# Kernel tuning notes

Measured on AMD Instinct MI355X. Metric: run time of the kernel, lower is better.

The kernel has to match this reference:

```python
import jax, jax.numpy as jnp
import numpy as np
import math

NUM_HEADS = 12


def setup_inputs() -> dict:
    key = jax.random.key(0)
    ks = jax.random.split(key, 9)
    R, L, B, E = 128, 512, 1, 768
    s = 1.0 / math.sqrt(E)
    return {
        "x": jax.random.normal(ks[0], (R, L, B, E), dtype=jnp.float32),
        "wq": jax.random.normal(ks[1], (E, E), dtype=jnp.float32) * s,
        "bq": jax.random.normal(ks[2], (E,), dtype=jnp.float32) * 0.02,
        "wk": jax.random.normal(ks[3], (E, E), dtype=jnp.float32) * s,
        "bk": jax.random.normal(ks[4], (E,), dtype=jnp.float32) * 0.02,
        "wv": jax.random.normal(ks[5], (E, E), dtype=jnp.float32) * s,
        "bv": jax.random.normal(ks[6], (E,), dtype=jnp.float32) * 0.02,
        "wo": jax.random.normal(ks[7], (E, E), dtype=jnp.float32) * s,
        "bo": jax.random.normal(ks[8], (E,), dtype=jnp.float32) * 0.02,
    }


def reference(x, wq, bq, wk, bk, wv, bv, wo, bo):
    # x: [num_rows, num_cols, batch, embed_dim]
    R, L, B, E = x.shape
    H = NUM_HEADS
    D = E // H
    # scaling = head_dim**-0.5 / sqrt(num_rows)  (align_scaling)
    scaling = (D ** -0.5) / math.sqrt(R)

    q = (x @ wq.T + bq).reshape(R, L, B, H, D) * scaling
    k = (x @ wk.T + bk).reshape(R, L, B, H, D)
    v = (x @ wv.T + bv).reshape(R, L, B, H, D)

    # row attention: contract over rows r and head_dim d -> logits [h, n, i, j]
    attn_weights = jnp.einsum("rinhd,rjnhd->hnij", q, k)
    attn_probs = jax.nn.softmax(attn_weights, axis=-1)

    context = jnp.einsum("hnij,rjnhd->rinhd", attn_probs, v)
    context = context.reshape(R, L, B, E)
    output = context @ wo.T + bo
    return (output, attn_probs)
```

## Files before the change

### kernel.cpp

```cpp
#include <hip/hip_runtime.h>
#include <hip/hip_bf16.h>

typedef unsigned short u16;
typedef u16   u16x4 __attribute__((ext_vector_type(4)));
typedef u16   u16x8 __attribute__((ext_vector_type(8)));
typedef short bf16x8 __attribute__((ext_vector_type(8)));
typedef float f32x4 __attribute__((ext_vector_type(4)));

#define R_    128
#define L_    512
#define E_    768
#define H_    12
#define RD_   8192
#define M_    65536
#define OUT0_N 50331648
#define PART_ 3145728

__device__ __forceinline__ u16 rne_bf16(float f) {
  unsigned u = __builtin_bit_cast(unsigned, f);
  u += 0x7FFFu + ((u >> 16) & 1u);
  return (u16)(u >> 16);
}

__device__ __forceinline__ void gload_lds16(const u16* g, u16* l) {
  __builtin_amdgcn_global_load_lds(
      (const __attribute__((address_space(1))) void*)g,
      (__attribute__((address_space(3))) void*)l, 16, 0, 0);
}

__device__ __forceinline__ int xcd_remap(int d, int nwg) {
  return (d & 7) * (nwg >> 3) + (d >> 3);
}

__device__ __forceinline__ void gemm_core256(
    const u16* __restrict__ Ab, const u16* __restrict__ Bb,
    const int lda, const int ldb, const int K,
    u16* sm, f32x4 acc[8][4])
{
  const int t    = threadIdx.x;
  const int lane = t & 63;
  const int w    = t >> 6;
  const int wm   = (w >> 2) << 7;
  const int wn   = (w & 3) << 6;
  const int frow = lane & 15;

  const int crow  = t >> 3;
  const int gslot = (t & 7) ^ (crow & 7);
  const u16* gA = Ab + (size_t)crow * lda + (gslot << 3);
  const u16* gB = Bb + (size_t)crow * ldb + (gslot << 3);
  const int stg = t << 3;

  const int rd0 = (((lane >> 4)    ) ^ (lane & 7)) << 3;
  const int rd1 = (((lane >> 4) | 4) ^ (lane & 7)) << 3;

#define STG_A(c_, buf_, ko_) \
  gload_lds16(gA + (ko_) + (size_t)((c_) << 6) * lda, (buf_) + ((c_) << 12) + stg)
#define STG_B(c_, buf_, ko_) \
  gload_lds16(gB + (ko_) + (size_t)((c_) << 6) * ldb, (buf_) + 16384 + ((c_) << 12) + stg)

  const int nt = K >> 6;
  STG_B(0, sm, 0); STG_B(1, sm, 0); STG_B(2, sm, 0); STG_B(3, sm, 0);
  STG_A(0, sm, 0); STG_A(2, sm, 0); STG_A(1, sm, 0); STG_A(3, sm, 0);
  asm volatile("s_waitcnt vmcnt(2)" ::: "memory");
  __builtin_amdgcn_s_barrier();

  for (int tt = 0; tt < nt; ++tt) {
    u16* bufc = sm + ((tt & 1) << 15);
    u16* bufn = sm + (((tt + 1) & 1) << 15);
    const bool st = (tt + 1 < nt);
    const int ko = (tt + 1) << 6;

    bf16x8 af[4], bff[4];
#pragma unroll
    for (int b = 0; b < 4; ++b)
      bff[b] = *(const bf16x8*)(bufc + 16384 + ((wn + b * 16 + frow) << 6) + rd0);
#pragma unroll
    for (int a = 0; a < 4; ++a)
      af[a] = *(const bf16x8*)(bufc + ((wm + a * 16 + frow) << 6) + rd0);
    if (st) { STG_B(0, bufn, ko); STG_B(1, bufn, ko); }
    __builtin_amdgcn_s_barrier();
    __builtin_amdgcn_s_setprio(1);
#pragma unroll
    for (int a = 0; a < 4; ++a)
#pragma unroll
      for (int b = 0; b < 4; ++b)
        acc[a][b] = __builtin_amdgcn_mfma_f32_16x16x32_bf16(af[a], bff[b], acc[a][b], 0, 0, 0);
    __builtin_amdgcn_s_setprio(0);
    if (st) asm volatile("s_waitcnt vmcnt(2)" ::: "memory");
    else    asm volatile("s_waitcnt vmcnt(0)" ::: "memory");
    __builtin_amdgcn_s_barrier();

#pragma unroll
    for (int a = 0; a < 4; ++a)
      af[a] = *(const bf16x8*)(bufc + ((wm + (a + 4) * 16 + frow) << 6) + rd0);
    if (st) { STG_B(2, bufn, ko); STG_B(3, bufn, ko); }
    __builtin_amdgcn_s_barrier();
    __builtin_amdgcn_s_setprio(1);
#pragma unroll
    for (int a = 0; a < 4; ++a)
#pragma unroll
      for (int b = 0; b < 4; ++b)
        acc[a + 4][b] = __builtin_amdgcn_mfma_f32_16x16x32_bf16(af[a], bff[b], acc[a + 4][b], 0, 0, 0);
    __builtin_amdgcn_s_setprio(0);
    __builtin_amdgcn_s_barrier();

#pragma unroll
    for (int b = 0; b < 4; ++b)
      bff[b] = *(const bf16x8*)(bufc + 16384 + ((wn + b * 16 + frow) << 6) + rd1);
#pragma unroll
    for (int a = 0; a < 4; ++a)
      af[a] = *(const bf16x8*)(bufc + ((wm + a * 16 + frow) << 6) + rd1);
    if (st) { STG_A(0, bufn, ko); STG_A(2, bufn, ko); }
    __builtin_amdgcn_s_barrier();
    __builtin_amdgcn_s_setprio(1);
#pragma unroll
    for (int a = 0; a < 4; ++a)
#pragma unroll
      for (int b = 0; b < 4; ++b)
        acc[a][b] = __builtin_amdgcn_mfma_f32_16x16x32_bf16(af[a], bff[b], acc[a][b], 0, 0, 0);
    __builtin_amdgcn_s_setprio(0);
    __builtin_amdgcn_s_barrier();

#pragma unroll
    for (int a = 0; a < 4; ++a)
      af[a] = *(const bf16x8*)(bufc + ((wm + (a + 4) * 16 + frow) << 6) + rd1);
    if (st) { STG_A(1, bufn, ko); STG_A(3, bufn, ko); }
    __builtin_amdgcn_s_barrier();
    __builtin_amdgcn_s_setprio(1);
#pragma unroll
    for (int a = 0; a < 4; ++a)
#pragma unroll
      for (int b = 0; b < 4; ++b)
        acc[a + 4][b] = __builtin_amdgcn_mfma_f32_16x16x32_bf16(af[a], bff[b], acc[a + 4][b], 0, 0, 0);
    __builtin_amdgcn_s_setprio(0);
    if (st) asm volatile("s_waitcnt vmcnt(2)" ::: "memory");
    __builtin_amdgcn_s_barrier();
  }
#undef STG_A
#undef STG_B
}

#define EPILOGUE_IDX256                           \
  const int lane = threadIdx.x & 63;              \
  const int w    = threadIdx.x >> 6;              \
  const int wm   = (w >> 2) << 7;                 \
  const int wn   = (w & 3) << 6;                  \
  const int row4 = (lane >> 4) << 2;              \
  const int coll = lane & 15;

#define ACC_INIT256                               \
  f32x4 acc[8][4];                                \
  {                                               \
    f32x4 zz = {0.0f, 0.0f, 0.0f, 0.0f};          \
    _Pragma("unroll")                             \
    for (int a = 0; a < 8; ++a)                   \
      _Pragma("unroll")                           \
      for (int b = 0; b < 4; ++b) acc[a][b] = zz; \
  }

__device__ __forceinline__ void gemm_core(
    const u16* __restrict__ Ab, const u16* __restrict__ Bb,
    const int lda, const int ldb, const int K,
    u16* sm, f32x4 acc[4][4])
{
  const int t    = threadIdx.x;
  const int lane = t & 63;
  const int w    = t >> 6;
  const int wm   = (w >> 1) << 6;
  const int wn   = (w & 1) << 6;
  const int frow = lane & 15;

  const int srow = (w << 3) + (lane >> 3);
  const int scol = ((lane & 7) ^ (lane >> 3)) << 3;
  const u16* gA = Ab + (size_t)srow * lda + scol;
  const u16* gB = Bb + (size_t)srow * ldb + scol;
  const int stg_l = (w << 9) + (lane << 3);

#pragma unroll
  for (int j = 0; j < 4; ++j) {
    gload_lds16(gA + (size_t)(j << 5) * lda, sm + (j << 11) + stg_l);
    gload_lds16(gB + (size_t)(j << 5) * ldb, sm + 8192 + (j << 11) + stg_l);
  }

  const int nt = K >> 6;
  for (int tt = 0; tt < nt; ++tt) {
    const int cur = tt & 1;
    u16* bufc = sm + (cur << 14);
    u16* bufn = sm + ((cur ^ 1) << 14);
    __builtin_amdgcn_s_barrier();
    if (tt + 1 < nt) {
      const u16* gA1 = gA + ((size_t)(tt + 1) << 6);
      const u16* gB1 = gB + ((size_t)(tt + 1) << 6);
#pragma unroll
      for (int j = 0; j < 4; ++j) {
        gload_lds16(gA1 + (size_t)(j << 5) * lda, bufn + (j << 11) + stg_l);
        gload_lds16(gB1 + (size_t)(j << 5) * ldb, bufn + 8192 + (j << 11) + stg_l);
      }
      asm volatile("s_waitcnt vmcnt(8)" ::: "memory");
    } else {
      asm volatile("s_waitcnt vmcnt(0)" ::: "memory");
    }
    __builtin_amdgcn_s_barrier();
    const u16* sA = bufc;
    const u16* sB = bufc + 8192;
#pragma unroll
    for (int kk = 0; kk < 2; ++kk) {
      const int rdcol = (((kk << 2) + (lane >> 4)) ^ (lane & 7)) << 3;
      bf16x8 af[4], bff[4];
#pragma unroll
      for (int a = 0; a < 4; ++a)
        af[a] = *(const bf16x8*)(sA + ((wm + a * 16 + frow) << 6) + rdcol);
#pragma unroll
      for (int b = 0; b < 4; ++b)
        bff[b] = *(const bf16x8*)(sB + ((wn + b * 16 + frow) << 6) + rdcol);
#pragma unroll
      for (int a = 0; a < 4; ++a)
#pragma unroll
        for (int b = 0; b < 4; ++b)
          acc[a][b] = __builtin_amdgcn_mfma_f32_16x16x32_bf16(af[a], bff[b], acc[a][b], 0, 0, 0);
    }
  }
}

#define EPILOGUE_IDX                              \
  const int lane = threadIdx.x & 63;              \
  const int w    = threadIdx.x >> 6;              \
  const int wm   = (w >> 1) << 6;                 \
  const int wn   = (w & 1) << 6;                  \
  const int row4 = (lane >> 4) << 2;              \
  const int coll = lane & 15;

#define ACC_INIT                                  \
  f32x4 acc[4][4];                                \
  {                                               \
    f32x4 zz = {0.0f, 0.0f, 0.0f, 0.0f};          \
    _Pragma("unroll")                             \
    for (int a = 0; a < 4; ++a)                   \
      _Pragma("unroll")                           \
      for (int b = 0; b < 4; ++b) acc[a][b] = zz; \
  }

__global__ __launch_bounds__(512) void k_gemm_qkv(
    const u16* __restrict__ xbf, const u16* __restrict__ wqkv,
    const float* __restrict__ bq, const float* __restrict__ bk,
    const float* __restrict__ bv,
    u16* __restrict__ qt, u16* __restrict__ kt, u16* __restrict__ vt2,
    const float scaling)
{
  __shared__ __align__(16) u16 smem[65536];
  const int d0 = blockIdx.x + 9 * blockIdx.y;
  const int l  = xcd_remap(d0, 2304);
  const int bn = l % 9;
  const int bm = l / 9;
  ACC_INIT256;
  gemm_core256(xbf + (size_t)bm * 256 * E_, wqkv + (size_t)bn * 256 * E_,
               E_, E_, E_, smem, acc);
  EPILOGUE_IDX256;
  const int which = bn / 3;
  const int c0 = (bn % 3) << 8;
  const float* bias = (which == 0) ? bq : (which == 1) ? bk : bv;

  if (which < 2) {
    u16* dst = (which == 0) ? qt : kt;
    const float mult = (which == 0) ? scaling : 1.0f;
#pragma unroll
    for (int a = 0; a < 8; ++a) {
#pragma unroll
      for (int b = 0; b < 4; ++b) {
        const int c = c0 + wn + b * 16 + coll;
        const int h = c >> 6, d = c & 63;
        const float bias_v = bias[c];
#pragma unroll
        for (int r = 0; r < 4; ++r) {
          const int m = (bm << 8) + wm + a * 16 + row4 + r;
          const int rr = m >> 9, i = m & 511;
          const float v = (acc[a][b][r] + bias_v) * mult;
          dst[((size_t)(h * 512 + i) << 13) + (rr << 6) + d] = rne_bf16(v);
        }
      }
    }
  } else {
    const int rr = bm >> 1;
    const int j0 = (bm & 1) << 8;
    const int wq4 = w & 3;
    for (int p = 0; p < 4; ++p) {
      __syncthreads();
      if (wq4 == p) {
#pragma unroll
        for (int a = 0; a < 8; ++a) {
          const int ml = wm + a * 16 + row4;
#pragma unroll
          for (int b = 0; b < 4; ++b) {
            const int c = c0 + wn + b * 16 + coll;
            const int nl = b * 16 + coll;
            const float bias_v = bias[c];
            u16x4 pk;
#pragma unroll
            for (int r = 0; r < 4; ++r) pk[r] = rne_bf16(acc[a][b][r] + bias_v);
            *(u16x4*)(smem + nl * 264 + ml) = pk;
          }
        }
      }
      __syncthreads();
      for (int idx = threadIdx.x; idx < 2048; idx += 512) {
        const int nl = idx >> 5, seg = idx & 31;
        const int c = c0 + (p << 6) + nl;
        const int h = c >> 6, d = c & 63;
        u16x8 vdat = *(const u16x8*)(smem + nl * 264 + (seg << 3));
        *(u16x8*)(vt2 + ((size_t)((h << 13) + (rr << 6) + d) << 9) + j0 + (seg << 3)) = vdat;
      }
    }
  }
}

__global__ __launch_bounds__(256) void k_gemm_logits(
    const u16* __restrict__ qt, const u16* __restrict__ kt,
    float* __restrict__ lgp)
{
  __shared__ __align__(16) u16 smem[32768];
  const int d0 = blockIdx.x + 4 * blockIdx.y + 16 * blockIdx.z;
  const int l  = xcd_remap(d0, 768);
  const int bm = l & 3, bn = (l >> 2) & 3;
  const int hk = l >> 4;
  const int h  = hk >> 2, ks = hk & 3;
  ACC_INIT;
  const u16* A = qt + ((size_t)h << 22) + ((size_t)bm << 20) + (ks << 11);
  const u16* B = kt + ((size_t)h << 22) + ((size_t)bn << 20) + (ks << 11);
  gemm_core(A, B, RD_, RD_, 2048, smem, acc);
  EPILOGUE_IDX;
  float* dst = lgp + ((size_t)(ks * 12 + h) << 18);
#pragma unroll
  for (int a = 0; a < 4; ++a)
#pragma unroll
    for (int b = 0; b < 4; ++b) {
      const int j = bn * 128 + wn + b * 16 + coll;
#pragma unroll
      for (int r = 0; r < 4; ++r) {
        const int i = bm * 128 + wm + a * 16 + row4 + r;
        dst[((size_t)i << 9) + j] = acc[a][b][r];
      }
    }
}

__global__ __launch_bounds__(256) void k_softmax(
    const float* __restrict__ lgp, float* __restrict__ probs,
    u16* __restrict__ pbf)
{
  const int row = blockIdx.x;
  const size_t base = (size_t)row << 9;
  const int t = threadIdx.x;
  const int lane = t & 63, w = t >> 6;
  float x0 = (lgp[base + t]       + lgp[PART_ + base + t])
           + (lgp[2 * (size_t)PART_ + base + t]       + lgp[3 * (size_t)PART_ + base + t]);
  float x1 = (lgp[base + t + 256] + lgp[PART_ + base + t + 256])
           + (lgp[2 * (size_t)PART_ + base + t + 256] + lgp[3 * (size_t)PART_ + base + t + 256]);
  float m = fmaxf(x0, x1);
#pragma unroll
  for (int off = 32; off > 0; off >>= 1) m = fmaxf(m, __shfl_xor(m, off, 64));
  __shared__ float red[8];
  if (lane == 0) red[w] = m;
  __syncthreads();
  m = fmaxf(fmaxf(red[0], red[1]), fmaxf(red[2], red[3]));
  float e0 = __expf(x0 - m), e1 = __expf(x1 - m);
  float s = e0 + e1;
#pragma unroll
  for (int off = 32; off > 0; off >>= 1) s += __shfl_xor(s, off, 64);
  if (lane == 0) red[4 + w] = s;
  __syncthreads();
  s = (red[4] + red[5]) + (red[6] + red[7]);
  const float inv = 1.0f / s;
  const float p0 = e0 * inv, p1 = e1 * inv;
  probs[base + t] = p0;
  probs[base + t + 256] = p1;
  pbf[base + t]       = rne_bf16(p0);
  pbf[base + t + 256] = rne_bf16(p1);
}

__global__ __launch_bounds__(512) void k_gemm_ctx(
    const u16* __restrict__ pbf, const u16* __restrict__ vt2,
    u16* __restrict__ ctx)
{
  __shared__ __align__(16) u16 smem[65536];
  const int d0 = blockIdx.x + (blockIdx.y << 6);
  const int l  = xcd_remap(d0, 768);
  const int bm = l & 1, bn = (l >> 1) & 31, h = l >> 6;
  ACC_INIT256;
  const u16* A = pbf + ((size_t)h << 18) + ((size_t)bm << 17);
  const u16* B = vt2 + ((size_t)h << 22) + ((size_t)bn << 17);
  gemm_core256(A, B, 512, 512, 512, smem, acc);
  EPILOGUE_IDX256;
#pragma unroll
  for (int a = 0; a < 8; ++a)
#pragma unroll
    for (int b = 0; b < 4; ++b) {
      const int n = (bn << 8) + wn + b * 16 + coll;
      const int rr = n >> 6, d = n & 63;
#pragma unroll
      for (int r = 0; r < 4; ++r) {
        const int i = (bm << 8) + wm + a * 16 + row4 + r;
        ctx[(size_t)((rr << 9) + i) * E_ + (h << 6) + d] = rne_bf16(acc[a][b][r]);
      }
    }
}

__global__ __launch_bounds__(512) void k_gemm_out(
    const u16* __restrict__ ctx, const u16* __restrict__ wob,
    const float* __restrict__ bo, float* __restrict__ out0)
{
  __shared__ __align__(16) u16 smem[65536];
  const int d0 = blockIdx.x + 3 * blockIdx.y;
  const int l  = xcd_remap(d0, 768);
  const int bn = l % 3;
  const int bm = l / 3;
  ACC_INIT256;
  gemm_core256(ctx + (size_t)bm * 256 * E_, wob + (size_t)bn * 256 * E_,
               E_, E_, E_, smem, acc);
  EPILOGUE_IDX256;
#pragma unroll
  for (int a = 0; a < 8; ++a)
#pragma unroll
    for (int b = 0; b < 4; ++b) {
      const int n = (bn << 8) + wn + b * 16 + coll;
      const float bias_v = bo[n];
#pragma unroll
      for (int r = 0; r < 4; ++r) {
        const int m = (bm << 8) + wm + a * 16 + row4 + r;
        out0[(size_t)m * E_ + n] = acc[a][b][r] + bias_v;
      }
    }
}

__device__ __forceinline__ u16x4 cvt4(float4 v) {
  u16x4 o;
  o.x = rne_bf16(v.x); o.y = rne_bf16(v.y);
  o.z = rne_bf16(v.z); o.w = rne_bf16(v.w);
  return o;
}

__global__ __launch_bounds__(256) void k_cvt_all(
    const float4* __restrict__ x,
    const float4* __restrict__ wq, const float4* __restrict__ wk,
    const float4* __restrict__ wv, const float4* __restrict__ wo,
    u16x4* __restrict__ xbf, u16x4* __restrict__ wqkv, u16x4* __restrict__ wob)
{
  const int n4x = OUT0_N / 4;
  const int n4w = (E_ * E_) / 4;
  const int stride = gridDim.x * blockDim.x;
  for (int i = blockIdx.x * blockDim.x + threadIdx.x; i < n4x; i += stride) {
    xbf[i] = cvt4(x[i]);
    if (i < n4w) {
      wqkv[i]          = cvt4(wq[i]);
      wqkv[n4w + i]    = cvt4(wk[i]);
      wqkv[2 * n4w + i] = cvt4(wv[i]);
      wob[i]           = cvt4(wo[i]);
    }
  }
}

__global__ void k_ws_too_small(float* out0) {
  if (threadIdx.x == 0 && blockIdx.x == 0) out0[0] = 1.0e9f;
}

extern "C" void kernel_launch(void* const* d_in, const int* in_sizes, int n_in,
                              void* d_out, int out_size, void* d_ws, size_t ws_size,
                              hipStream_t stream)
{
  const float* x  = (const float*)d_in[0];
  const float* wq = (const float*)d_in[1];
  const float* bq = (const float*)d_in[2];
  const float* wk = (const float*)d_in[3];
  const float* bk = (const float*)d_in[4];
  const float* wv = (const float*)d_in[5];
  const float* bv = (const float*)d_in[6];
  const float* wo = (const float*)d_in[7];
  const float* bo = (const float*)d_in[8];

  float* out0 = (float*)d_out;
  float* outp = out0 + (size_t)OUT0_N;

  const size_t off_xbf   = 0;
  const size_t off_qt    = 100663296;
  const size_t off_kt    = 201326592;
  const size_t off_vt    = 301989888;
  const size_t off_pbf   = 402653184;
  const size_t off_wqkv  = 408944640;
  const size_t off_wob   = 412483584;
  const size_t need      = 413663232;

  if (ws_size < need) {
    k_ws_too_small<<<1, 64, 0, stream>>>(out0);
    return;
  }

  char* ws = (char*)d_ws;
  u16* xbf  = (u16*)(ws + off_xbf);
  float* lgp = (float*)(ws + off_xbf);
  u16* qt   = (u16*)(ws + off_qt);
  u16* kt   = (u16*)(ws + off_kt);
  u16* vt2  = (u16*)(ws + off_vt);
  u16* pbf  = (u16*)(ws + off_pbf);
  u16* wqkv = (u16*)(ws + off_wqkv);
  u16* wob  = (u16*)(ws + off_wob);

  const float scaling = 0.011048543456039806f;

  k_cvt_all<<<2048, 256, 0, stream>>>((const float4*)x,
                                      (const float4*)wq, (const float4*)wk,
                                      (const float4*)wv, (const float4*)wo,
                                      (u16x4*)xbf, (u16x4*)wqkv, (u16x4*)wob);
  k_gemm_qkv<<<dim3(9, 256), 512, 0, stream>>>(xbf, wqkv, bq, bk, bv,
                                               qt, kt, vt2, scaling);
  k_gemm_logits<<<dim3(4, 4, 48), 256, 0, stream>>>(qt, kt, lgp);
  k_softmax<<<6144, 256, 0, stream>>>(lgp, outp, pbf);
  k_gemm_ctx<<<dim3(64, 12), 512, 0, stream>>>(pbf, vt2, xbf );
  k_gemm_out<<<dim3(3, 256), 512, 0, stream>>>(xbf, wob, bo, out0);
}
```

Before: 601.8 us.

## Use 16 waves per 256x256 GEMM tile with simpler double-buffered K loop

The 256x256 GEMM core goes from 8 waves, each computing 128x64, to 16 waves (1024 threads), each computing 64x64. Accumulator registers per wave are halved. The finely interleaved staged load/compute schedule is replaced by one prefetch of the next K tile at the top of each iteration, followed by two k-substeps of MFMA. The aim is more waves to hide latency with less register pressure, at the cost of losing the fine-grained load/compute interleave, and launch_bounds(1024,4) may squeeze registers.

```diff
diff --git a/kernel.cpp b/kernel.cpp
--- a/kernel.cpp
+++ b/kernel.cpp
@@ -35,12 +35,12 @@
 __device__ __forceinline__ void gemm_core256(
     const u16* __restrict__ Ab, const u16* __restrict__ Bb,
     const int lda, const int ldb, const int K,
-    u16* sm, f32x4 acc[8][4])
+    u16* sm, f32x4 acc[4][4])
 {
   const int t    = threadIdx.x;
   const int lane = t & 63;
   const int w    = t >> 6;
-  const int wm   = (w >> 2) << 7;
+  const int wm   = (w >> 2) << 6;
   const int wn   = (w & 3) << 6;
   const int frow = lane & 15;
 
@@ -54,86 +54,47 @@
   const int rd1 = (((lane >> 4) | 4) ^ (lane & 7)) << 3;
 
 #define STG_A(c_, buf_, ko_) \
-  gload_lds16(gA + (ko_) + (size_t)((c_) << 6) * lda, (buf_) + ((c_) << 12) + stg)
+  gload_lds16(gA + (ko_) + (size_t)((c_) << 7) * lda, (buf_) + ((c_) << 13) + stg)
 #define STG_B(c_, buf_, ko_) \
-  gload_lds16(gB + (ko_) + (size_t)((c_) << 6) * ldb, (buf_) + 16384 + ((c_) << 12) + stg)
+  gload_lds16(gB + (ko_) + (size_t)((c_) << 7) * ldb, (buf_) + 16384 + ((c_) << 13) + stg)
 
   const int nt = K >> 6;
-  STG_B(0, sm, 0); STG_B(1, sm, 0); STG_B(2, sm, 0); STG_B(3, sm, 0);
-  STG_A(0, sm, 0); STG_A(2, sm, 0); STG_A(1, sm, 0); STG_A(3, sm, 0);
-  asm volatile("s_waitcnt vmcnt(2)" ::: "memory");
+  STG_A(0, sm, 0); STG_A(1, sm, 0); STG_B(0, sm, 0); STG_B(1, sm, 0);
+  asm volatile("s_waitcnt vmcnt(0)" ::: "memory");
   __builtin_amdgcn_s_barrier();
 
   for (int tt = 0; tt < nt; ++tt) {
     u16* bufc = sm + ((tt & 1) << 15);
     u16* bufn = sm + (((tt + 1) & 1) << 15);
     const bool st = (tt + 1 < nt);
-    const int ko = (tt + 1) << 6;
+    if (st) {
+      const int ko = (tt + 1) << 6;
+      STG_A(0, bufn, ko); STG_A(1, bufn, ko);
+      STG_B(0, bufn, ko); STG_B(1, bufn, ko);
+      asm volatile("s_waitcnt vmcnt(4)" ::: "memory");
+    } else {
+      asm volatile("s_waitcnt vmcnt(0)" ::: "memory");
+    }
+    __builtin_amdgcn_s_barrier();
 
     bf16x8 af[4], bff[4];
 #pragma unroll
-    for (int b = 0; b < 4; ++b)
-      bff[b] = *(const bf16x8*)(bufc + 16384 + ((wn + b * 16 + frow) << 6) + rd0);
-#pragma unroll
-    for (int a = 0; a < 4; ++a)
-      af[a] = *(const bf16x8*)(bufc + ((wm + a * 16 + frow) << 6) + rd0);
-    if (st) { STG_B(0, bufn, ko); STG_B(1, bufn, ko); }
-    __builtin_amdgcn_s_barrier();
-    __builtin_amdgcn_s_setprio(1);
-#pragma unroll
-    for (int a = 0; a < 4; ++a)
+    for (int kk = 0; kk < 2; ++kk) {
+      const int rdk = kk ? rd1 : rd0;
+#pragma unroll
+      for (int a = 0; a < 4; ++a)
+        af[a] = *(const bf16x8*)(bufc + ((wm + a * 16 + frow) << 6) + rdk);
 #pragma unroll
       for (int b = 0; b < 4; ++b)
-        acc[a][b] = __builtin_amdgcn_mfma_f32_16x16x32_bf16(af[a], bff[b], acc[a][b], 0, 0, 0);
-    __builtin_amdgcn_s_setprio(0);
-    if (st) asm volatile("s_waitcnt vmcnt(2)" ::: "memory");
-    else    asm volatile("s_waitcnt vmcnt(0)" ::: "memory");
-    __builtin_amdgcn_s_barrier();
-
-#pragma unroll
-    for (int a = 0; a < 4; ++a)
-      af[a] = *(const bf16x8*)(bufc + ((wm + (a + 4) * 16 + frow) << 6) + rd0);
-    if (st) { STG_B(2, bufn, ko); STG_B(3, bufn, ko); }
-    __builtin_amdgcn_s_barrier();
-    __builtin_amdgcn_s_setprio(1);
-#pragma unroll
-    for (int a = 0; a < 4; ++a)
-#pragma unroll
-      for (int b = 0; b < 4; ++b)
-        acc[a + 4][b] = __builtin_amdgcn_mfma_f32_16x16x32_bf16(af[a], bff[b], acc[a + 4][b], 0, 0, 0);
-    __builtin_amdgcn_s_setprio(0);
-    __builtin_amdgcn_s_barrier();
-
-#pragma unroll
-    for (int b = 0; b < 4; ++b)
-      bff[b] = *(const bf16x8*)(bufc + 16384 + ((wn + b * 16 + frow) << 6) + rd1);
-#pragma unroll
-    for (int a = 0; a < 4; ++a)
-      af[a] = *(const bf16x8*)(bufc + ((wm + a * 16 + frow) << 6) + rd1);
-    if (st) { STG_A(0, bufn, ko); STG_A(2, bufn, ko); }
-    __builtin_amdgcn_s_barrier();
-    __builtin_amdgcn_s_setprio(1);
-#pragma unroll
-    for (int a = 0; a < 4; ++a)
-#pragma unroll
-      for (int b = 0; b < 4; ++b)
-        acc[a][b] = __builtin_amdgcn_mfma_f32_16x16x32_bf16(af[a], bff[b], acc[a][b], 0, 0, 0);
-    __builtin_amdgcn_s_setprio(0);
-    __builtin_amdgcn_s_barrier();
-
-#pragma unroll
-    for (int a = 0; a < 4; ++a)
-      af[a] = *(const bf16x8*)(bufc + ((wm + (a + 4) * 16 + frow) << 6) + rd1);
-    if (st) { STG_A(1, bufn, ko); STG_A(3, bufn, ko); }
-    __builtin_amdgcn_s_barrier();
-    __builtin_amdgcn_s_setprio(1);
-#pragma unroll
-    for (int a = 0; a < 4; ++a)
-#pragma unroll
-      for (int b = 0; b < 4; ++b)
-        acc[a + 4][b] = __builtin_amdgcn_mfma_f32_16x16x32_bf16(af[a], bff[b], acc[a + 4][b], 0, 0, 0);
-    __builtin_amdgcn_s_setprio(0);
-    if (st) asm volatile("s_waitcnt vmcnt(2)" ::: "memory");
+        bff[b] = *(const bf16x8*)(bufc + 16384 + ((wn + b * 16 + frow) << 6) + rdk);
+      __builtin_amdgcn_s_setprio(1);
+#pragma unroll
+      for (int a = 0; a < 4; ++a)
+#pragma unroll
+        for (int b = 0; b < 4; ++b)
+          acc[a][b] = __builtin_amdgcn_mfma_f32_16x16x32_bf16(af[a], bff[b], acc[a][b], 0, 0, 0);
+      __builtin_amdgcn_s_setprio(0);
+    }
     __builtin_amdgcn_s_barrier();
   }
 #undef STG_A
@@ -143,17 +104,17 @@
 #define EPILOGUE_IDX256                           \
   const int lane = threadIdx.x & 63;              \
   const int w    = threadIdx.x >> 6;              \
-  const int wm   = (w >> 2) << 7;                 \
+  const int wm   = (w >> 2) << 6;                 \
   const int wn   = (w & 3) << 6;                  \
   const int row4 = (lane >> 4) << 2;              \
   const int coll = lane & 15;
 
 #define ACC_INIT256                               \
-  f32x4 acc[8][4];                                \
+  f32x4 acc[4][4];                                \
   {                                               \
     f32x4 zz = {0.0f, 0.0f, 0.0f, 0.0f};          \
     _Pragma("unroll")                             \
-    for (int a = 0; a < 8; ++a)                   \
+    for (int a = 0; a < 4; ++a)                   \
       _Pragma("unroll")                           \
       for (int b = 0; b < 4; ++b) acc[a][b] = zz; \
   }
@@ -240,7 +201,7 @@
       for (int b = 0; b < 4; ++b) acc[a][b] = zz; \
   }
 
-__global__ __launch_bounds__(512) void k_gemm_qkv(
+__global__ __launch_bounds__(1024, 4) void k_gemm_qkv(
     const u16* __restrict__ xbf, const u16* __restrict__ wqkv,
     const float* __restrict__ bq, const float* __restrict__ bk,
     const float* __restrict__ bv,
@@ -264,7 +225,7 @@
     u16* dst = (which == 0) ? qt : kt;
     const float mult = (which == 0) ? scaling : 1.0f;
 #pragma unroll
-    for (int a = 0; a < 8; ++a) {
+    for (int a = 0; a < 4; ++a) {
 #pragma unroll
       for (int b = 0; b < 4; ++b) {
         const int c = c0 + wn + b * 16 + coll;
@@ -287,7 +248,7 @@
       __syncthreads();
       if (wq4 == p) {
 #pragma unroll
-        for (int a = 0; a < 8; ++a) {
+        for (int a = 0; a < 4; ++a) {
           const int ml = wm + a * 16 + row4;
 #pragma unroll
           for (int b = 0; b < 4; ++b) {
@@ -302,7 +263,7 @@
         }
       }
       __syncthreads();
-      for (int idx = threadIdx.x; idx < 2048; idx += 512) {
+      for (int idx = threadIdx.x; idx < 2048; idx += 1024) {
         const int nl = idx >> 5, seg = idx & 31;
         const int c = c0 + (p << 6) + nl;
         const int h = c >> 6, d = c & 63;
@@ -376,7 +337,7 @@
   pbf[base + t + 256] = rne_bf16(p1);
 }
 
-__global__ __launch_bounds__(512) void k_gemm_ctx(
+__global__ __launch_bounds__(1024, 4) void k_gemm_ctx(
     const u16* __restrict__ pbf, const u16* __restrict__ vt2,
     u16* __restrict__ ctx)
 {
@@ -390,7 +351,7 @@
   gemm_core256(A, B, 512, 512, 512, smem, acc);
   EPILOGUE_IDX256;
 #pragma unroll
-  for (int a = 0; a < 8; ++a)
+  for (int a = 0; a < 4; ++a)
 #pragma unroll
     for (int b = 0; b < 4; ++b) {
       const int n = (bn << 8) + wn + b * 16 + coll;
@@ -403,7 +364,7 @@
     }
 }
 
-__global__ __launch_bounds__(512) void k_gemm_out(
+__global__ __launch_bounds__(1024, 4) void k_gemm_out(
     const u16* __restrict__ ctx, const u16* __restrict__ wob,
     const float* __restrict__ bo, float* __restrict__ out0)
 {
@@ -417,7 +378,7 @@
                E_, E_, E_, smem, acc);
   EPILOGUE_IDX256;
 #pragma unroll
-  for (int a = 0; a < 8; ++a)
+  for (int a = 0; a < 4; ++a)
 #pragma unroll
     for (int b = 0; b < 4; ++b) {
       const int n = (bn << 8) + wn + b * 16 + coll;
@@ -508,10 +469,10 @@
                                       (const float4*)wq, (const float4*)wk,
                                       (const float4*)wv, (const float4*)wo,
                                       (u16x4*)xbf, (u16x4*)wqkv, (u16x4*)wob);
-  k_gemm_qkv<<<dim3(9, 256), 512, 0, stream>>>(xbf, wqkv, bq, bk, bv,
-                                               qt, kt, vt2, scaling);
+  k_gemm_qkv<<<dim3(9, 256), 1024, 0, stream>>>(xbf, wqkv, bq, bk, bv,
+                                                qt, kt, vt2, scaling);
   k_gemm_logits<<<dim3(4, 4, 48), 256, 0, stream>>>(qt, kt, lgp);
   k_softmax<<<6144, 256, 0, stream>>>(lgp, outp, pbf);
-  k_gemm_ctx<<<dim3(64, 12), 512, 0, stream>>>(pbf, vt2, xbf );
-  k_gemm_out<<<dim3(3, 256), 512, 0, stream>>>(xbf, wob, bo, out0);
-}
+  k_gemm_ctx<<<dim3(64, 12), 1024, 0, stream>>>(pbf, vt2, xbf );
+  k_gemm_out<<<dim3(3, 256), 1024, 0, stream>>>(xbf, wob, bo, out0);
+}
```

Result: slower. 644.2 us (+7.1%).
